# Performance work log

Measured on AMD Instinct MI355X. Metric: run time of the kernel, lower is better.

## Reference

```python
import jax, jax.numpy as jnp
import numpy as np

NUM_ELEMENTS = 100
EMBED_DIM = 256
HIDDEN_DIM = 512
NUM_HEADS = 8
NUM_MASKS = 1
NUM_GAUSSIANS = 50
RBF_RADIUS = 12.0
N_NODES = 20000
N_EDGES = 400000


def setup_inputs() -> dict:
    key = jax.random.key(0)
    ks = jax.random.split(key, 10)
    anum = jax.random.randint(ks[0], (N_NODES,), 0, NUM_ELEMENTS)
    edge_index = jax.random.randint(ks[1], (2, N_EDGES), 0, N_NODES)
    edge_to_src = jax.random.randint(ks[2], (N_EDGES,), 0, N_EDGES)
    dist = jax.random.uniform(ks[3], (N_EDGES,), jnp.float32) * RBF_RADIUS
    # learned parameters (init scales follow reset_parameters)
    emb_table = jax.random.normal(ks[4], (NUM_ELEMENTS ** 2, EMBED_DIM), jnp.float32)
    s_gate = np.sqrt(3.0 / 2.50663)
    gate_W = jax.random.uniform(ks[5], (HIDDEN_DIM, NUM_GAUSSIANS), jnp.float32, -s_gate, s_gate)
    in_dim = EMBED_DIM + NUM_GAUSSIANS
    s_emb = np.sqrt(3.0 / EMBED_DIM)
    W_emb = jax.random.uniform(ks[6], (HIDDEN_DIM, EMBED_DIM), jnp.float32, -s_emb, s_emb)
    W_rbf = jax.random.uniform(ks[7], (HIDDEN_DIM, NUM_GAUSSIANS), jnp.float32, -s_gate, s_gate)
    W_in = jnp.concatenate([W_emb, W_rbf], axis=1)  # [H, emb+G]
    b_in = jnp.zeros((HIDDEN_DIM,), jnp.float32)
    s_out = np.sqrt(1.0 / HIDDEN_DIM)
    W_out = jax.random.uniform(ks[8], (NUM_HEADS * NUM_MASKS, HIDDEN_DIM), jnp.float32, -s_out, s_out)
    b_out = jnp.zeros((NUM_HEADS * NUM_MASKS,), jnp.float32)
    return {"anum": anum, "edge_index": edge_index, "edge_to_src": edge_to_src,
            "dist": dist, "emb_table": emb_table, "gate_W": gate_W,
            "W_in": W_in, "b_in": b_in, "W_out": W_out, "b_out": b_out}


def _gaussian_smearing(dist):
    offset = jnp.linspace(0.0, RBF_RADIUS, NUM_GAUSSIANS, dtype=dist.dtype)
    coeff = -0.5 / (offset[1] - offset[0]) ** 2
    d = dist[:, None] - offset[None, :]  # [E, G]
    return jnp.exp(coeff * d * d)


def reference(anum, edge_index, edge_to_src, dist, emb_table, gate_W, W_in, b_in, W_out, b_out):
    rbf = _gaussian_smearing(dist)                                  # [E, G]
    pair_idx = anum[edge_index[0]] + NUM_ELEMENTS * anum[edge_index[1]]  # [E]
    emb = emb_table[pair_idx]                                       # [E, D]
    x = jnp.concatenate([emb[edge_to_src], rbf], axis=-1)           # [E, D+G]
    gate = rbf @ gate_W.T                                           # [E, H]
    h = jax.nn.silu(x @ W_in.T + b_in) * gate                       # gated ResMLP hidden
    att_bias = h @ W_out.T + b_out                                  # [E, heads*masks]
    att_bias = att_bias.reshape(dist.shape[0], NUM_HEADS, NUM_MASKS)
    return jnp.transpose(att_bias, (2, 1, 0))                       # [masks, heads, E]
```

## Files before the change

kernel.cpp:

```cpp
#include <hip/hip_runtime.h>
#include <hip/hip_bf16.h>

typedef unsigned short u16;
typedef unsigned int   uint;
typedef __attribute__((ext_vector_type(8))) short bf16x8;
typedef __attribute__((ext_vector_type(4))) float f32x4;

constexpr int NELEM = 100;
constexpr int EMBED = 256;
constexpr int HID   = 512;
constexpr int KX    = 306;
constexpr int G     = 50;
constexpr int M     = 64;
constexpr int THREADS = 512;

constexpr int WB_ELEMS = 32 * 10 * 64 * 8;
constexpr int GB_ELEMS = 32 * 2 * 64 * 8;
constexpr int OB_ELEMS = 16 * 64 * 8;
constexpr int WEIGHT_ELEMS = WB_ELEMS + GB_ELEMS + OB_ELEMS;

__device__ __forceinline__ u16 f2bf(float x) {
    uint u = __float_as_uint(x);
    u = (u + 0x7fffu + ((u >> 16) & 1u)) >> 16;
    return (u16)u;
}
__device__ __forceinline__ uint pk2(float a, float b) {
    __hip_bfloat162 h = __float22bfloat162_rn(make_float2(a, b));
    return *reinterpret_cast<uint*>(&h);
}
__device__ __forceinline__ float bflo(uint u) { return __uint_as_float(u << 16); }
__device__ __forceinline__ float bfhi(uint u) { return __uint_as_float(u & 0xffff0000u); }
__device__ __forceinline__ float silu(float p) {
    return p * __builtin_amdgcn_rcpf(1.f + __expf(-p));
}
__device__ __forceinline__ f32x4 mfma16(bf16x8 a, bf16x8 b, f32x4 c) {
    return __builtin_amdgcn_mfma_f32_16x16x32_bf16(a, b, c, 0, 0, 0);
}
__device__ __forceinline__ void load_lds16(const u16* g, u16* l) {
    __builtin_amdgcn_global_load_lds(
        (const __attribute__((address_space(1))) uint*)g,
        (__attribute__((address_space(3))) uint*)l, 16, 0, 0);
}

__global__ void prep_all_kernel(const float* __restrict__ W_in,
                                const float* __restrict__ gate_W,
                                const float* __restrict__ W_out,
                                const float* __restrict__ b_in,
                                const float* __restrict__ table,
                                u16* __restrict__ Wb,
                                u16* __restrict__ Gb,
                                u16* __restrict__ Ob,
                                uint* __restrict__ Eb4,
                                int nconv, int do_conv) {
    int idx = blockIdx.x * 256 + threadIdx.x;
    if (idx < WB_ELEMS) {
        int j = idx & 7, lane = (idx >> 3) & 63, kn = idx >> 9;
        int ks = kn % 10, nt = kn / 10;
        int h = nt * 16 + (lane & 15);
        int k = ks * 32 + (lane >> 4) * 8 + j;
        float v = (k < KX) ? W_in[h * KX + k] : ((k == KX) ? b_in[h] : 0.f);
        Wb[idx] = f2bf(v);
    } else if (idx < WB_ELEMS + GB_ELEMS) {
        int i2 = idx - WB_ELEMS;
        int j = i2 & 7, lane = (i2 >> 3) & 63, kn = i2 >> 9;
        int ks = kn & 1, nt = kn >> 1;
        int h = nt * 16 + (lane & 15);
        int g = ks * 32 + (lane >> 4) * 8 + j;
        Gb[i2] = f2bf((g < G) ? gate_W[h * G + g] : 0.f);
    } else if (idx < WEIGHT_ELEMS) {
        int i2 = idx - WB_ELEMS - GB_ELEMS;
        int j = i2 & 7, lane = (i2 >> 3) & 63, s = i2 >> 9;
        int m = lane & 15, q = lane >> 4;
        int hid = s * 32 + (j >> 2) * 16 + q * 4 + (j & 3);
        Ob[i2] = f2bf((m < 8) ? W_out[m * HID + hid] : 0.f);
    } else if (do_conv) {
        int i = idx - WEIGHT_ELEMS;
        if (i < nconv) {
            const float4* s4 = (const float4*)(table + i * 8);
            float4 v0 = s4[0], v1 = s4[1];
            uint4 w;
            w.x = pk2(v0.x, v0.y); w.y = pk2(v0.z, v0.w);
            w.z = pk2(v1.x, v1.y); w.w = pk2(v1.z, v1.w);
            ((uint4*)Eb4)[i] = w;
        }
    }
}

template <bool BF16_TABLE>
__global__ __launch_bounds__(THREADS, 4)
void pair_embed_kernel(const int* __restrict__ anum,
                       const int* __restrict__ edge_index,
                       const int* __restrict__ edge_to_src,
                       const float* __restrict__ dist,
                       const float* __restrict__ emb_table,
                       const u16* __restrict__ Eb,
                       const float* __restrict__ b_out,
                       const u16* __restrict__ Wb,
                       const u16* __restrict__ Gb,
                       const u16* __restrict__ Ob,
                       float* __restrict__ out,
                       int E) {
    __shared__ __align__(16) u16 smem[10 * 4 * 64 * 8];
    __shared__ int   rowbase[M];
    __shared__ float dste[M];
    u16*   afrag = smem;
    float* redf  = (float*)smem;

    const int t  = threadIdx.x;
    const int e0 = blockIdx.x * M;
    const int wave = t >> 6, lane = t & 63;
    const int col = lane & 15, quad = lane >> 4;

    if (t < M) {
        int eg = e0 + t;
        int pair = 0; float d = 0.f;
        if (eg < E) {
            int src = edge_to_src[eg];
            pair = anum[edge_index[src]] + NELEM * anum[edge_index[E + src]];
            d = dist[eg];
        }
        rowbase[t] = pair * EMBED;
        dste[t]    = d;
    }
    __syncthreads();

    {
        if (BF16_TABLE) {
            #pragma unroll
            for (int mt = 0; mt < 4; ++mt) {
                int rb = rowbase[mt * 16 + col];
                const u16* g = Eb + rb + wave * 32 + quad * 8;
                load_lds16(g, &afrag[((wave * 4 + mt) * 64 + lane) * 8]);
            }
        } else {
            #pragma unroll 1
            for (int mt = 0; mt < 4; ++mt) {
                int rb = rowbase[mt * 16 + col];
                const float4* src = (const float4*)(emb_table + rb + wave * 32 + quad * 8);
                float4 v0 = src[0], v1 = src[1];
                uint4 w;
                w.x = pk2(v0.x, v0.y); w.y = pk2(v0.z, v0.w);
                w.z = pk2(v1.x, v1.y); w.w = pk2(v1.z, v1.w);
                *(uint4*)&afrag[((wave * 4 + mt) * 64 + lane) * 8] = w;
            }
        }
        {
            const float sp    = 12.0f / 49.0f;
            const float coeff = -0.5f / (sp * sp);
            int ksr = 8 + (wave & 1), mtr = wave >> 1;
            float d  = dste[mtr * 16 + col];
            int   k0 = ksr * 32 + quad * 8;
            float f[8];
            #pragma unroll
            for (int j = 0; j < 8; ++j) {
                int k = k0 + j;
                int g = k - EMBED;
                float dd = d - sp * (float)g;
                f[j] = (g < G) ? __expf(coeff * dd * dd) : ((k == KX) ? 1.f : 0.f);
            }
            uint4 w;
            w.x = pk2(f[0], f[1]); w.y = pk2(f[2], f[3]);
            w.z = pk2(f[4], f[5]); w.w = pk2(f[6], f[7]);
            *(uint4*)&afrag[((ksr * 4 + mtr) * 64 + lane) * 8] = w;
        }
    }
    __syncthreads();

    const f32x4 z4 = {0.f, 0.f, 0.f, 0.f};
    f32x4 oacc[4] = {z4, z4, z4, z4};

    #pragma unroll
    for (int nh = 0; nh < 2; ++nh) {
        uint gp[2][4][2];
        {
            f32x4 gacc[2][4];
            #pragma unroll
            for (int ntl = 0; ntl < 2; ++ntl)
                #pragma unroll
                for (int mt = 0; mt < 4; ++mt) gacc[ntl][mt] = z4;
            #pragma unroll
            for (int ks = 0; ks < 2; ++ks) {
                bf16x8 a[4];
                #pragma unroll
                for (int mt = 0; mt < 4; ++mt)
                    a[mt] = *(const bf16x8*)&afrag[(((8 + ks) * 4 + mt) * 64 + lane) * 8];
                #pragma unroll
                for (int ntl = 0; ntl < 2; ++ntl) {
                    int ntg = wave * 4 + nh * 2 + ntl;
                    bf16x8 g = *(const bf16x8*)&Gb[((ntg * 2 + ks) * 64 + lane) * 8];
                    #pragma unroll
                    for (int mt = 0; mt < 4; ++mt)
                        gacc[ntl][mt] = mfma16(g, a[mt], gacc[ntl][mt]);
                }
            }
            #pragma unroll
            for (int ntl = 0; ntl < 2; ++ntl)
                #pragma unroll
                for (int mt = 0; mt < 4; ++mt) {
                    gp[ntl][mt][0] = pk2(gacc[ntl][mt][0], gacc[ntl][mt][1]);
                    gp[ntl][mt][1] = pk2(gacc[ntl][mt][2], gacc[ntl][mt][3]);
                }
        }

        f32x4 acc[2][4];
        #pragma unroll
        for (int ntl = 0; ntl < 2; ++ntl)
            #pragma unroll
            for (int mt = 0; mt < 4; ++mt) acc[ntl][mt] = z4;
        const u16* wb0 = &Wb[(((wave * 4 + nh * 2 + 0) * 10) * 64 + lane) * 8];
        const u16* wb1 = &Wb[(((wave * 4 + nh * 2 + 1) * 10) * 64 + lane) * 8];
        #pragma unroll 2
        for (int ks = 0; ks < 10; ++ks) {
            bf16x8 a[4];
            #pragma unroll
            for (int mt = 0; mt < 4; ++mt)
                a[mt] = *(const bf16x8*)&afrag[((ks * 4 + mt) * 64 + lane) * 8];
            bf16x8 w0 = *(const bf16x8*)&wb0[ks * 512];
            #pragma unroll
            for (int mt = 0; mt < 4; ++mt)
                acc[0][mt] = mfma16(w0, a[mt], acc[0][mt]);
            bf16x8 w1 = *(const bf16x8*)&wb1[ks * 512];
            #pragma unroll
            for (int mt = 0; mt < 4; ++mt)
                acc[1][mt] = mfma16(w1, a[mt], acc[1][mt]);
        }

        bf16x8 obf = *(const bf16x8*)&Ob[(((wave << 1) | nh) * 64 + lane) * 8];
        #pragma unroll
        for (int mt = 0; mt < 4; ++mt) {
            uint4 hq;
            hq.x = pk2(silu(acc[0][mt][0]) * bflo(gp[0][mt][0]),
                       silu(acc[0][mt][1]) * bfhi(gp[0][mt][0]));
            hq.y = pk2(silu(acc[0][mt][2]) * bflo(gp[0][mt][1]),
                       silu(acc[0][mt][3]) * bfhi(gp[0][mt][1]));
            hq.z = pk2(silu(acc[1][mt][0]) * bflo(gp[1][mt][0]),
                       silu(acc[1][mt][1]) * bfhi(gp[1][mt][0]));
            hq.w = pk2(silu(acc[1][mt][2]) * bflo(gp[1][mt][1]),
                       silu(acc[1][mt][3]) * bfhi(gp[1][mt][1]));
            oacc[mt] = mfma16(obf, *(bf16x8*)&hq, oacc[mt]);
        }
    }
    __syncthreads();

    #pragma unroll
    for (int mt = 0; mt < 4; ++mt)
        *(f32x4*)&redf[((wave * 4 + mt) * 64 + lane) * 4] = oacc[mt];
    __syncthreads();

    {
        int head = t >> 6, el = t & 63;
        int mt = el >> 4, c = el & 15;
        int l  = (head >> 2) * 16 + c;
        int r  = head & 3;
        float s = 0.f;
        #pragma unroll
        for (int w = 0; w < 8; ++w)
            s += redf[((w * 4 + mt) * 64 + l) * 4 + r];
        int eg = e0 + el;
        if (eg < E) out[head * E + eg] = s + b_out[head];
    }
}

extern "C" void kernel_launch(void* const* d_in, const int* in_sizes, int n_in,
                              void* d_out, int out_size, void* d_ws, size_t ws_size,
                              hipStream_t stream) {
    const int*   anum        = (const int*)d_in[0];
    const int*   edge_index  = (const int*)d_in[1];
    const int*   edge_to_src = (const int*)d_in[2];
    const float* dist        = (const float*)d_in[3];
    const float* emb_table   = (const float*)d_in[4];
    const float* gate_W      = (const float*)d_in[5];
    const float* W_in        = (const float*)d_in[6];
    const float* b_in        = (const float*)d_in[7];
    const float* W_out       = (const float*)d_in[8];
    const float* b_out       = (const float*)d_in[9];
    const int E   = in_sizes[3];
    const int TBL = in_sizes[4];

    u16* Wb = (u16*)d_ws;
    u16* Gb = Wb + WB_ELEMS;
    u16* Ob = Gb + GB_ELEMS;
    u16* Eb = Ob + OB_ELEMS;

    const size_t need_bf16 = (size_t)(WEIGHT_ELEMS + TBL) * sizeof(u16);
    const bool use_bf16_table = ws_size >= need_bf16;

    const int nconv = TBL / 8;
    const int total = WEIGHT_ELEMS + (use_bf16_table ? nconv : 0);
    prep_all_kernel<<<(total + 255) / 256, 256, 0, stream>>>(
        W_in, gate_W, W_out, b_in, emb_table,
        Wb, Gb, Ob, (uint*)Eb, nconv, use_bf16_table ? 1 : 0);

    const int nblocks = (E + M - 1) / M;
    if (use_bf16_table) {
        pair_embed_kernel<true><<<nblocks, THREADS, 0, stream>>>(
            anum, edge_index, edge_to_src, dist, emb_table, Eb,
            b_out, Wb, Gb, Ob, (float*)d_out, E);
    } else {
        pair_embed_kernel<false><<<nblocks, THREADS, 0, stream>>>(
            anum, edge_index, edge_to_src, dist, emb_table, Eb,
            b_out, Wb, Gb, Ob, (float*)d_out, E);
    }
}
```

Baseline: 264.3 us.

## Precompute per-pair W_emb projection table and gather it instead of embedding GEMM

```diff
diff --git a/kernel.cpp b/kernel.cpp
--- a/kernel.cpp
+++ b/kernel.cpp
@@ -36,71 +36,134 @@
 __device__ __forceinline__ f32x4 mfma16(bf16x8 a, bf16x8 b, f32x4 c) {
     return __builtin_amdgcn_mfma_f32_16x16x32_bf16(a, b, c, 0, 0, 0);
 }
-__device__ __forceinline__ void load_lds16(const u16* g, u16* l) {
-    __builtin_amdgcn_global_load_lds(
-        (const __attribute__((address_space(1))) uint*)g,
-        (__attribute__((address_space(3))) uint*)l, 16, 0, 0);
-}
-
-__global__ void prep_all_kernel(const float* __restrict__ W_in,
-                                const float* __restrict__ gate_W,
-                                const float* __restrict__ W_out,
-                                const float* __restrict__ b_in,
-                                const float* __restrict__ table,
-                                u16* __restrict__ Wb,
-                                u16* __restrict__ Gb,
-                                u16* __restrict__ Ob,
-                                uint* __restrict__ Eb4,
-                                int nconv, int do_conv) {
-    int idx = blockIdx.x * 256 + threadIdx.x;
-    if (idx < WB_ELEMS) {
-        int j = idx & 7, lane = (idx >> 3) & 63, kn = idx >> 9;
-        int ks = kn % 10, nt = kn / 10;
-        int h = nt * 16 + (lane & 15);
-        int k = ks * 32 + (lane >> 4) * 8 + j;
-        float v = (k < KX) ? W_in[h * KX + k] : ((k == KX) ? b_in[h] : 0.f);
-        Wb[idx] = f2bf(v);
-    } else if (idx < WB_ELEMS + GB_ELEMS) {
-        int i2 = idx - WB_ELEMS;
-        int j = i2 & 7, lane = (i2 >> 3) & 63, kn = i2 >> 9;
-        int ks = kn & 1, nt = kn >> 1;
-        int h = nt * 16 + (lane & 15);
-        int g = ks * 32 + (lane >> 4) * 8 + j;
-        Gb[i2] = f2bf((g < G) ? gate_W[h * G + g] : 0.f);
-    } else if (idx < WEIGHT_ELEMS) {
-        int i2 = idx - WB_ELEMS - GB_ELEMS;
-        int j = i2 & 7, lane = (i2 >> 3) & 63, s = i2 >> 9;
-        int m = lane & 15, q = lane >> 4;
-        int hid = s * 32 + (j >> 2) * 16 + q * 4 + (j & 3);
-        Ob[i2] = f2bf((m < 8) ? W_out[m * HID + hid] : 0.f);
-    } else if (do_conv) {
-        int i = idx - WEIGHT_ELEMS;
-        if (i < nconv) {
-            const float4* s4 = (const float4*)(table + i * 8);
-            float4 v0 = s4[0], v1 = s4[1];
-            uint4 w;
+
+__global__ __launch_bounds__(THREADS)
+void prep_kernel(const float* __restrict__ W_in,
+                 const float* __restrict__ gate_W,
+                 const float* __restrict__ W_out,
+                 const float* __restrict__ b_in,
+                 const float* __restrict__ table,
+                 u16* __restrict__ Wb,
+                 u16* __restrict__ Gb,
+                 u16* __restrict__ Ob,
+                 float* __restrict__ hpreF,
+                 u16*   __restrict__ hpreH,
+                 int npair, int nprep, int mode) {
+    __shared__ __align__(16) u16 af[8 * 4 * 64 * 8];
+    const int bid = blockIdx.x;
+    const int t   = threadIdx.x;
+
+    if (bid < nprep) {
+        int idx = bid * THREADS + t;
+        if (idx < WB_ELEMS) {
+            int j = idx & 7, lane = (idx >> 3) & 63, kn = idx >> 9;
+            int ks = kn % 10, nt = kn / 10;
+            int h = nt * 16 + (lane & 15);
+            int k = ks * 32 + (lane >> 4) * 8 + j;
+            float v = (k < KX) ? W_in[h * KX + k] : ((k == KX) ? b_in[h] : 0.f);
+            Wb[idx] = f2bf(v);
+        } else if (idx < WB_ELEMS + GB_ELEMS) {
+            int i2 = idx - WB_ELEMS;
+            int j = i2 & 7, lane = (i2 >> 3) & 63, kn = i2 >> 9;
+            int ks = kn & 1, nt = kn >> 1;
+            int h = nt * 16 + (lane & 15);
+            int g = ks * 32 + (lane >> 4) * 8 + j;
+            Gb[i2] = f2bf((g < G) ? gate_W[h * G + g] : 0.f);
+        } else if (idx < WEIGHT_ELEMS) {
+            int i2 = idx - WB_ELEMS - GB_ELEMS;
+            int j = i2 & 7, lane = (i2 >> 3) & 63, s = i2 >> 9;
+            int m = lane & 15, q = lane >> 4;
+            int hid = s * 32 + (j >> 2) * 16 + q * 4 + (j & 3);
+            Ob[i2] = f2bf((m < 8) ? W_out[m * HID + hid] : 0.f);
+        }
+        return;
+    }
+
+    const int pb = bid - nprep;
+    const int p0 = pb * M;
+    const int wave = t >> 6, lane = t & 63;
+    const int col = lane & 15, quad = lane >> 4;
+
+    #pragma unroll
+    for (int mt = 0; mt < 4; ++mt) {
+        int p = p0 + mt * 16 + col;
+        uint4 w = {0u, 0u, 0u, 0u};
+        if (p < npair) {
+            const float* s = table + p * EMBED + wave * 32 + quad * 8;
+            float4 v0 = ((const float4*)s)[0], v1 = ((const float4*)s)[1];
             w.x = pk2(v0.x, v0.y); w.y = pk2(v0.z, v0.w);
             w.z = pk2(v1.x, v1.y); w.w = pk2(v1.z, v1.w);
-            ((uint4*)Eb4)[i] = w;
-        }
-    }
-}
-
-template <bool BF16_TABLE>
+        }
+        *(uint4*)&af[((wave * 4 + mt) * 64 + lane) * 8] = w;
+    }
+    __syncthreads();
+
+    const f32x4 z4 = {0.f, 0.f, 0.f, 0.f};
+    #pragma unroll
+    for (int nh = 0; nh < 2; ++nh) {
+        f32x4 acc[2][4];
+        #pragma unroll
+        for (int ntl = 0; ntl < 2; ++ntl)
+            #pragma unroll
+            for (int mt = 0; mt < 4; ++mt) acc[ntl][mt] = z4;
+        #pragma unroll 2
+        for (int ks = 0; ks < 8; ++ks) {
+            bf16x8 a[4];
+            #pragma unroll
+            for (int mt = 0; mt < 4; ++mt)
+                a[mt] = *(const bf16x8*)&af[((ks * 4 + mt) * 64 + lane) * 8];
+            #pragma unroll
+            for (int ntl = 0; ntl < 2; ++ntl) {
+                int h = (wave * 4 + nh * 2 + ntl) * 16 + col;
+                int k0 = ks * 32 + quad * 8;
+                const float* wsrc = W_in + h * KX + k0;
+                float2 u0 = ((const float2*)wsrc)[0];
+                float2 u1 = ((const float2*)wsrc)[1];
+                float2 u2 = ((const float2*)wsrc)[2];
+                float2 u3 = ((const float2*)wsrc)[3];
+                uint4 wf;
+                wf.x = pk2(u0.x, u0.y); wf.y = pk2(u1.x, u1.y);
+                wf.z = pk2(u2.x, u2.y); wf.w = pk2(u3.x, u3.y);
+                #pragma unroll
+                for (int mt = 0; mt < 4; ++mt)
+                    acc[ntl][mt] = mfma16(*(bf16x8*)&wf, a[mt], acc[ntl][mt]);
+            }
+        }
+        #pragma unroll
+        for (int ntl = 0; ntl < 2; ++ntl)
+            #pragma unroll
+            for (int mt = 0; mt < 4; ++mt) {
+                int p = p0 + mt * 16 + col;
+                if (p < npair) {
+                    int hb = (wave * 4 + nh * 2 + ntl) * 16 + quad * 4;
+                    if (mode == 2) {
+                        *(f32x4*)(hpreF + (size_t)p * HID + hb) = acc[ntl][mt];
+                    } else {
+                        uint2 o;
+                        o.x = pk2(acc[ntl][mt][0], acc[ntl][mt][1]);
+                        o.y = pk2(acc[ntl][mt][2], acc[ntl][mt][3]);
+                        *(uint2*)(hpreH + (size_t)p * HID + hb) = o;
+                    }
+                }
+            }
+    }
+}
+
+template <bool F32H>
 __global__ __launch_bounds__(THREADS, 4)
-void pair_embed_kernel(const int* __restrict__ anum,
-                       const int* __restrict__ edge_index,
-                       const int* __restrict__ edge_to_src,
-                       const float* __restrict__ dist,
-                       const float* __restrict__ emb_table,
-                       const u16* __restrict__ Eb,
-                       const float* __restrict__ b_out,
-                       const u16* __restrict__ Wb,
-                       const u16* __restrict__ Gb,
-                       const u16* __restrict__ Ob,
-                       float* __restrict__ out,
-                       int E) {
-    __shared__ __align__(16) u16 smem[10 * 4 * 64 * 8];
+void pair_embed_pre(const int* __restrict__ anum,
+                    const int* __restrict__ edge_index,
+                    const int* __restrict__ edge_to_src,
+                    const float* __restrict__ dist,
+                    const float* __restrict__ hpreF,
+                    const u16*   __restrict__ hpreH,
+                    const float* __restrict__ b_out,
+                    const u16* __restrict__ Wb,
+                    const u16* __restrict__ Gb,
+                    const u16* __restrict__ Ob,
+                    float* __restrict__ out,
+                    int E) {
+    __shared__ __align__(16) u16 smem[16384];
     __shared__ int   rowbase[M];
     __shared__ float dste[M];
     u16*   afrag = smem;
@@ -119,30 +182,190 @@
             pair = anum[edge_index[src]] + NELEM * anum[edge_index[E + src]];
             d = dist[eg];
         }
+        rowbase[t] = pair * HID;
+        dste[t]    = d;
+    }
+    __syncthreads();
+
+    int rbm[4];
+    #pragma unroll
+    for (int mt = 0; mt < 4; ++mt) rbm[mt] = rowbase[mt * 16 + col];
+
+    f32x4 hp[2][4];
+    uint2 hph[2][4];
+    #pragma unroll
+    for (int mt = 0; mt < 4; ++mt) {
+        int base = rbm[mt] + (wave * 4) * 16 + quad * 4;
+        if (F32H) {
+            const float* p = hpreF + base;
+            hp[0][mt] = *(const f32x4*)p;
+            hp[1][mt] = *(const f32x4*)(p + 16);
+        } else {
+            const u16* p = hpreH + base;
+            hph[0][mt] = *(const uint2*)p;
+            hph[1][mt] = *(const uint2*)(p + 16);
+        }
+    }
+
+    {
+        const float sp    = 12.0f / 49.0f;
+        const float coeff = -0.5f / (sp * sp);
+        int ks = wave & 1, mtr = wave >> 1;
+        float d  = dste[mtr * 16 + col];
+        int   g0 = ks * 32 + quad * 8;
+        float f[8];
+        #pragma unroll
+        for (int j = 0; j < 8; ++j) {
+            int g = g0 + j;
+            float dd = d - sp * (float)g;
+            f[j] = (g < G) ? __expf(coeff * dd * dd) : ((g == G) ? 1.f : 0.f);
+        }
+        uint4 w;
+        w.x = pk2(f[0], f[1]); w.y = pk2(f[2], f[3]);
+        w.z = pk2(f[4], f[5]); w.w = pk2(f[6], f[7]);
+        *(uint4*)&afrag[((ks * 4 + mtr) * 64 + lane) * 8] = w;
+    }
+    __syncthreads();
+
+    const f32x4 z4 = {0.f, 0.f, 0.f, 0.f};
+    f32x4 oacc[4] = {z4, z4, z4, z4};
+
+    #pragma unroll
+    for (int nh = 0; nh < 2; ++nh) {
+        if (nh == 1) {
+            #pragma unroll
+            for (int mt = 0; mt < 4; ++mt) {
+                int base = rbm[mt] + (wave * 4 + 2) * 16 + quad * 4;
+                if (F32H) {
+                    const float* p = hpreF + base;
+                    hp[0][mt] = *(const f32x4*)p;
+                    hp[1][mt] = *(const f32x4*)(p + 16);
+                } else {
+                    const u16* p = hpreH + base;
+                    hph[0][mt] = *(const uint2*)p;
+                    hph[1][mt] = *(const uint2*)(p + 16);
+                }
+            }
+        }
+        f32x4 acc[2][4], gacc[2][4];
+        #pragma unroll
+        for (int ntl = 0; ntl < 2; ++ntl)
+            #pragma unroll
+            for (int mt = 0; mt < 4; ++mt) {
+                gacc[ntl][mt] = z4;
+                if (F32H) {
+                    acc[ntl][mt] = hp[ntl][mt];
+                } else {
+                    uint2 v = hph[ntl][mt];
+                    f32x4 a = {bflo(v.x), bfhi(v.x), bflo(v.y), bfhi(v.y)};
+                    acc[ntl][mt] = a;
+                }
+            }
+
+        const u16* gb = &Gb[((wave * 4 + nh * 2) * 2 * 64 + lane) * 8];
+        const u16* wb = &Wb[(((wave * 4 + nh * 2) * 10 + 8) * 64 + lane) * 8];
+        #pragma unroll
+        for (int ks = 0; ks < 2; ++ks) {
+            bf16x8 a[4];
+            #pragma unroll
+            for (int mt = 0; mt < 4; ++mt)
+                a[mt] = *(const bf16x8*)&afrag[((ks * 4 + mt) * 64 + lane) * 8];
+            bf16x8 g0f = *(const bf16x8*)&gb[ks * 512];
+            bf16x8 w0f = *(const bf16x8*)&wb[ks * 512];
+            bf16x8 g1f = *(const bf16x8*)&gb[1024 + ks * 512];
+            bf16x8 w1f = *(const bf16x8*)&wb[5120 + ks * 512];
+            #pragma unroll
+            for (int mt = 0; mt < 4; ++mt) gacc[0][mt] = mfma16(g0f, a[mt], gacc[0][mt]);
+            #pragma unroll
+            for (int mt = 0; mt < 4; ++mt) acc[0][mt]  = mfma16(w0f, a[mt], acc[0][mt]);
+            #pragma unroll
+            for (int mt = 0; mt < 4; ++mt) gacc[1][mt] = mfma16(g1f, a[mt], gacc[1][mt]);
+            #pragma unroll
+            for (int mt = 0; mt < 4; ++mt) acc[1][mt]  = mfma16(w1f, a[mt], acc[1][mt]);
+        }
+
+        bf16x8 obf = *(const bf16x8*)&Ob[(((wave << 1) | nh) * 64 + lane) * 8];
+        #pragma unroll
+        for (int mt = 0; mt < 4; ++mt) {
+            uint4 hq;
+            hq.x = pk2(silu(acc[0][mt][0]) * gacc[0][mt][0],
+                       silu(acc[0][mt][1]) * gacc[0][mt][1]);
+            hq.y = pk2(silu(acc[0][mt][2]) * gacc[0][mt][2],
+                       silu(acc[0][mt][3]) * gacc[0][mt][3]);
+            hq.z = pk2(silu(acc[1][mt][0]) * gacc[1][mt][0],
+                       silu(acc[1][mt][1]) * gacc[1][mt][1]);
+            hq.w = pk2(silu(acc[1][mt][2]) * gacc[1][mt][2],
+                       silu(acc[1][mt][3]) * gacc[1][mt][3]);
+            oacc[mt] = mfma16(obf, *(bf16x8*)&hq, oacc[mt]);
+        }
+    }
+    __syncthreads();
+
+    #pragma unroll
+    for (int mt = 0; mt < 4; ++mt)
+        *(f32x4*)&redf[((wave * 4 + mt) * 64 + lane) * 4] = oacc[mt];
+    __syncthreads();
+
+    {
+        int head = t >> 6, el = t & 63;
+        int mt = el >> 4, c = el & 15;
+        int l  = (head >> 2) * 16 + c;
+        int r  = head & 3;
+        float s = 0.f;
+        #pragma unroll
+        for (int w = 0; w < 8; ++w)
+            s += redf[((w * 4 + mt) * 64 + l) * 4 + r];
+        int eg = e0 + el;
+        if (eg < E) out[head * E + eg] = s + b_out[head];
+    }
+}
+
+__global__ __launch_bounds__(THREADS, 4)
+void pair_embed_old(const int* __restrict__ anum,
+                    const int* __restrict__ edge_index,
+                    const int* __restrict__ edge_to_src,
+                    const float* __restrict__ dist,
+                    const float* __restrict__ emb_table,
+                    const float* __restrict__ b_out,
+                    const u16* __restrict__ Wb,
+                    const u16* __restrict__ Gb,
+                    const u16* __restrict__ Ob,
+                    float* __restrict__ out,
+                    int E) {
+    __shared__ __align__(16) u16 smem[10 * 4 * 64 * 8];
+    __shared__ int   rowbase[M];
+    __shared__ float dste[M];
+    u16*   afrag = smem;
+    float* redf  = (float*)smem;
+
+    const int t  = threadIdx.x;
+    const int e0 = blockIdx.x * M;
+    const int wave = t >> 6, lane = t & 63;
+    const int col = lane & 15, quad = lane >> 4;
+
+    if (t < M) {
+        int eg = e0 + t;
+        int pair = 0; float d = 0.f;
+        if (eg < E) {
+            int src = edge_to_src[eg];
+            pair = anum[edge_index[src]] + NELEM * anum[edge_index[E + src]];
+            d = dist[eg];
+        }
         rowbase[t] = pair * EMBED;
         dste[t]    = d;
     }
     __syncthreads();
 
     {
-        if (BF16_TABLE) {
-            #pragma unroll
-            for (int mt = 0; mt < 4; ++mt) {
-                int rb = rowbase[mt * 16 + col];
-                const u16* g = Eb + rb + wave * 32 + quad * 8;
-                load_lds16(g, &afrag[((wave * 4 + mt) * 64 + lane) * 8]);
-            }
-        } else {
-            #pragma unroll 1
-            for (int mt = 0; mt < 4; ++mt) {
-                int rb = rowbase[mt * 16 + col];
-                const float4* src = (const float4*)(emb_table + rb + wave * 32 + quad * 8);
-                float4 v0 = src[0], v1 = src[1];
-                uint4 w;
-                w.x = pk2(v0.x, v0.y); w.y = pk2(v0.z, v0.w);
-                w.z = pk2(v1.x, v1.y); w.w = pk2(v1.z, v1.w);
-                *(uint4*)&afrag[((wave * 4 + mt) * 64 + lane) * 8] = w;
-            }
+        #pragma unroll 1
+        for (int mt = 0; mt < 4; ++mt) {
+            int rb = rowbase[mt * 16 + col];
+            const float4* src = (const float4*)(emb_table + rb + wave * 32 + quad * 8);
+            float4 v0 = src[0], v1 = src[1];
+            uint4 w;
+            w.x = pk2(v0.x, v0.y); w.y = pk2(v0.z, v0.w);
+            w.z = pk2(v1.x, v1.y); w.w = pk2(v1.z, v1.w);
+            *(uint4*)&afrag[((wave * 4 + mt) * 64 + lane) * 8] = w;
         }
         {
             const float sp    = 12.0f / 49.0f;
@@ -274,31 +497,38 @@
     const float* b_in        = (const float*)d_in[7];
     const float* W_out       = (const float*)d_in[8];
     const float* b_out       = (const float*)d_in[9];
-    const int E   = in_sizes[3];
-    const int TBL = in_sizes[4];
+    const int E     = in_sizes[3];
+    const int TBL   = in_sizes[4];
+    const int NPAIR = TBL / EMBED;
 
     u16* Wb = (u16*)d_ws;
     u16* Gb = Wb + WB_ELEMS;
     u16* Ob = Gb + GB_ELEMS;
-    u16* Eb = Ob + OB_ELEMS;
-
-    const size_t need_bf16 = (size_t)(WEIGHT_ELEMS + TBL) * sizeof(u16);
-    const bool use_bf16_table = ws_size >= need_bf16;
-
-    const int nconv = TBL / 8;
-    const int total = WEIGHT_ELEMS + (use_bf16_table ? nconv : 0);
-    prep_all_kernel<<<(total + 255) / 256, 256, 0, stream>>>(
+    char* hbase = (char*)d_ws + (size_t)WEIGHT_ELEMS * 2;
+
+    const size_t need32 = (size_t)WEIGHT_ELEMS * 2 + (size_t)NPAIR * HID * 4;
+    const size_t need16 = (size_t)WEIGHT_ELEMS * 2 + (size_t)NPAIR * HID * 2;
+    const int mode = (ws_size >= need32) ? 2 : ((ws_size >= need16) ? 1 : 0);
+
+    const int nprep = (WEIGHT_ELEMS + THREADS - 1) / THREADS;
+    const int npb   = (NPAIR + M - 1) / M;
+    const int grid  = nprep + (mode ? npb : 0);
+    prep_kernel<<<grid, THREADS, 0, stream>>>(
         W_in, gate_W, W_out, b_in, emb_table,
-        Wb, Gb, Ob, (uint*)Eb, nconv, use_bf16_table ? 1 : 0);
+        Wb, Gb, Ob, (float*)hbase, (u16*)hbase, NPAIR, nprep, mode);
 
     const int nblocks = (E + M - 1) / M;
-    if (use_bf16_table) {
-        pair_embed_kernel<true><<<nblocks, THREADS, 0, stream>>>(
-            anum, edge_index, edge_to_src, dist, emb_table, Eb,
+    if (mode == 2) {
+        pair_embed_pre<true><<<nblocks, THREADS, 0, stream>>>(
+            anum, edge_index, edge_to_src, dist, (const float*)hbase, (const u16*)hbase,
+            b_out, Wb, Gb, Ob, (float*)d_out, E);
+    } else if (mode == 1) {
+        pair_embed_pre<false><<<nblocks, THREADS, 0, stream>>>(
+            anum, edge_index, edge_to_src, dist, (const float*)hbase, (const u16*)hbase,
             b_out, Wb, Gb, Ob, (float*)d_out, E);
     } else {
-        pair_embed_kernel<false><<<nblocks, THREADS, 0, stream>>>(
-            anum, edge_index, edge_to_src, dist, emb_table, Eb,
+        pair_embed_old<<<nblocks, THREADS, 0, stream>>>(
+            anum, edge_index, edge_to_src, dist, emb_table,
             b_out, Wb, Gb, Ob, (float*)d_out, E);
     }
 }
```

Measured after the change: 287.8 us. +8.9%, slower.
